# Kernel tuning notes

Hardware: AMD Instinct MI355X
Metric: run time of the kernel (lower is better)

## Reference

```python
import jax, jax.numpy as jnp
import numpy as np
import math


def setup_inputs() -> dict:
    key = jax.random.key(0)
    ks = jax.random.split(key, 8)
    B, L, d_model, d_state, d_conv, expand = 2, 512, 1024, 64, 4, 2
    d_inner = expand * d_model  # 2048
    x = jax.random.normal(ks[0], (B, L, d_model), jnp.float32)
    in_proj_w = jax.random.normal(ks[1], (d_model, 2 * d_inner), jnp.float32) * (d_model ** -0.5)
    conv_w = jax.random.normal(ks[2], (d_inner, 1, d_conv), jnp.float32) * (d_conv ** -0.5)
    conv_b = jnp.zeros((d_inner,), jnp.float32)
    x_proj_w = jax.random.normal(ks[3], (d_inner, 2 * d_state + 1), jnp.float32) * (d_inner ** -0.5)
    dt_w = jax.random.normal(ks[4], (1, d_inner), jnp.float32)
    # dt bias init: softplus^{-1} of dt ~ LogUniform(dt_min, dt_max)
    dt = jnp.exp(jax.random.uniform(ks[5], (d_inner,)) * (math.log(0.1) - math.log(0.001)) + math.log(0.001))
    dt_b = dt + jnp.log(-jnp.expm1(-dt))
    A_log = jnp.broadcast_to(jnp.log(jnp.arange(1, d_state + 1, dtype=jnp.float32)), (d_inner, d_state)) + 0.0
    D = jnp.ones((d_inner,), jnp.float32)
    out_proj_w = jax.random.normal(ks[6], (d_inner, d_model), jnp.float32) * (d_inner ** -0.5)
    return {"x": x, "in_proj_w": in_proj_w, "conv_w": conv_w, "conv_b": conv_b,
            "x_proj_w": x_proj_w, "dt_w": dt_w, "dt_b": dt_b, "A_log": A_log,
            "D": D, "out_proj_w": out_proj_w}


def _mamba_forward(x, in_proj_w, conv_w, conv_b, x_proj_w, dt_w, dt_b, A_log, D, out_proj_w):
    Bsz, L, _ = x.shape
    d_inner, _, K = conv_w.shape
    d_state = A_log.shape[1]
    # in_proj -> split into x-branch and gate z
    xz = x @ in_proj_w                       # (B, L, 2*d_inner)
    xs, z = jnp.split(xz, 2, axis=-1)
    # depthwise causal conv1d (pad K-1 on the left == torch pad both + truncate to L)
    xc = jax.lax.conv_general_dilated(
        xs.transpose(0, 2, 1), conv_w, (1,), [(K - 1, 0)],
        dimension_numbers=("NCH", "OIH", "NCH"), feature_group_count=d_inner)
    xc = xc + conv_b[None, :, None]
    xs = jax.nn.silu(xc.transpose(0, 2, 1))  # (B, L, d_inner)
    # input-dependent SSM params
    xp = xs @ x_proj_w                       # (B, L, 2*d_state + 1)
    Bm = xp[..., :d_state]                   # (B, L, N)
    Cm = xp[..., d_state:2 * d_state]        # (B, L, N)
    dt_raw = xp[..., -1:]                    # (B, L, 1)
    dt = jax.nn.softplus(dt_raw @ dt_w + dt_b)  # (B, L, d_inner)
    A = -jnp.exp(A_log)                      # (d_inner, N)

    def step(state, inp):
        x_t, B_t, C_t, dt_t = inp            # (B,d), (B,N), (B,N), (B,d)
        dA = jnp.exp(dt_t[..., None] * A)    # (B, d, N)
        state = dA * state + (dt_t * x_t)[..., None] * B_t[:, None, :]
        y = jnp.einsum("bdn,bn->bd", state, C_t) + D * x_t
        return state, y

    init = jnp.zeros((Bsz, d_inner, d_state), xs.dtype)
    seq = (xs.transpose(1, 0, 2), Bm.transpose(1, 0, 2),
           Cm.transpose(1, 0, 2), dt.transpose(1, 0, 2))
    new_state, ys = jax.lax.scan(step, init, seq)
    y = ys.transpose(1, 0, 2)                # (B, L, d_inner)
    y = y * jax.nn.silu(z)
    out = y @ out_proj_w                     # (B, L, d_model)
    return out, new_state


def reference(x, in_proj_w, conv_w, conv_b, x_proj_w, dt_w, dt_b, A_log, D, out_proj_w):
    return _mamba_forward(x, in_proj_w, conv_w, conv_b, x_proj_w, dt_w, dt_b, A_log, D, out_proj_w)
```

## Files before the change

kernel.cpp:

```cpp
#include <hip/hip_runtime.h>
#include <hip/hip_bf16.h>


#define N_TOK   1024
#define SEQ_L   512
#define D_MODEL 1024
#define D_INNER 2048
#define D_STATE 64
#define D_XZ    4096
#define N_XP    129

typedef __attribute__((ext_vector_type(8))) short bf16x8;
typedef __attribute__((ext_vector_type(4))) float f32x4;

__device__ __forceinline__ unsigned short f2bf(float f) {
  __hip_bfloat16 h = __float2bfloat16(f);
  return *reinterpret_cast<unsigned short*>(&h);
}
__device__ __forceinline__ float bf16lo(unsigned int u) { return __uint_as_float(u << 16); }
__device__ __forceinline__ float bf16hi(unsigned int u) { return __uint_as_float(u & 0xffff0000u); }

__global__ __launch_bounds__(256) void transpose_bf16(
    const float* __restrict__ src, __hip_bfloat16* __restrict__ dst, int R, int C) {
  __shared__ float t[64][65];
  int c0 = blockIdx.x * 64, r0 = blockIdx.y * 64;
  int tc = threadIdx.x & 63, tg = threadIdx.x >> 6;
#pragma unroll
  for (int i = 0; i < 16; ++i) {
    int r = r0 + tg + i * 4, c = c0 + tc;
    t[tg + i * 4][tc] = (r < R && c < C) ? src[(size_t)r * C + c] : 0.f;
  }
  __syncthreads();
#pragma unroll
  for (int i = 0; i < 16; ++i) {
    int c = c0 + tg + i * 4, r = r0 + tc;
    if (c < C && r < R) dst[(size_t)c * R + r] = __float2bfloat16(t[tc][tg + i * 4]);
  }
}

template<int A_F32>
__global__ __launch_bounds__(256) void gemm_bf16_tn(
    const void* __restrict__ Av, const __hip_bfloat16* __restrict__ Bt,
    float* __restrict__ C, int M, int N, int K) {
  __shared__ short As[128][40];
  __shared__ short Bs[128][40];
  const int brow = blockIdx.y * 128, bcol = blockIdx.x * 128;
  const int tid = threadIdx.x;
  const int lane = tid & 63, wave = tid >> 6;
  const int wm = wave >> 1, wn = wave & 1;
  const int l15 = lane & 15, lk = lane >> 4;
  f32x4 acc[4][4] = {};
  for (int k0 = 0; k0 < K; k0 += 32) {
#pragma unroll
    for (int i = 0; i < 2; ++i) {
      int v = tid + i * 256;
      int r = v >> 2, kc = (v & 3) * 8;
      if (A_F32) {
        const float* Af = (const float*)Av;
        float4 f0 = *(const float4*)&Af[(size_t)(brow + r) * K + k0 + kc];
        float4 f1 = *(const float4*)&Af[(size_t)(brow + r) * K + k0 + kc + 4];
        bf16x8 h;
        h[0] = (short)f2bf(f0.x); h[1] = (short)f2bf(f0.y);
        h[2] = (short)f2bf(f0.z); h[3] = (short)f2bf(f0.w);
        h[4] = (short)f2bf(f1.x); h[5] = (short)f2bf(f1.y);
        h[6] = (short)f2bf(f1.z); h[7] = (short)f2bf(f1.w);
        *(bf16x8*)((char*)&As[0][0] + r * 80 + kc * 2) = h;
      } else {
        const __hip_bfloat16* Ab = (const __hip_bfloat16*)Av;
        *(bf16x8*)((char*)&As[0][0] + r * 80 + kc * 2) =
            *(const bf16x8*)&Ab[(size_t)(brow + r) * K + k0 + kc];
      }
      *(bf16x8*)((char*)&Bs[0][0] + r * 80 + kc * 2) =
          *(const bf16x8*)&Bt[(size_t)(bcol + r) * K + k0 + kc];
    }
    __syncthreads();
    bf16x8 af[4], bfr[4];
#pragma unroll
    for (int m = 0; m < 4; ++m)
      af[m] = *(const bf16x8*)((const char*)&As[0][0] + (wm * 64 + m * 16 + l15) * 80 + lk * 16);
#pragma unroll
    for (int n = 0; n < 4; ++n)
      bfr[n] = *(const bf16x8*)((const char*)&Bs[0][0] + (wn * 64 + n * 16 + l15) * 80 + lk * 16);
#pragma unroll
    for (int m = 0; m < 4; ++m)
#pragma unroll
      for (int n = 0; n < 4; ++n)
        acc[m][n] = __builtin_amdgcn_mfma_f32_16x16x32_bf16(af[m], bfr[n], acc[m][n], 0, 0, 0);
    __syncthreads();
  }
#pragma unroll
  for (int m = 0; m < 4; ++m) {
    int row = brow + wm * 64 + m * 16 + lk * 4;
#pragma unroll
    for (int n = 0; n < 4; ++n) {
      int col = bcol + wn * 64 + n * 16 + l15;
#pragma unroll
      for (int r = 0; r < 4; ++r)
        C[(size_t)(row + r) * N + col] = acc[m][n][r];
    }
  }
}

__global__ __launch_bounds__(256) void gemm_splitk(
    const __hip_bfloat16* __restrict__ A, const __hip_bfloat16* __restrict__ Bt,
    float* __restrict__ P, int M, int N, int K, int kchunk) {
  __shared__ short As[128][40];
  __shared__ short Bs[128][40];
  const int brow = blockIdx.y * 128, bcol = blockIdx.x * 128;
  const int kbase = blockIdx.z * kchunk;
  const int tid = threadIdx.x;
  const int lane = tid & 63, wave = tid >> 6;
  const int wm = wave >> 1, wn = wave & 1;
  const int l15 = lane & 15, lk = lane >> 4;
  f32x4 acc[4][4] = {};
  for (int k0 = kbase; k0 < kbase + kchunk; k0 += 32) {
#pragma unroll
    for (int i = 0; i < 2; ++i) {
      int v = tid + i * 256;
      int r = v >> 2, kc = (v & 3) * 8;
      *(bf16x8*)((char*)&As[0][0] + r * 80 + kc * 2) =
          *(const bf16x8*)&A[(size_t)(brow + r) * K + k0 + kc];
      bf16x8 bv = {};
      if ((bcol + r) < N)
        bv = *(const bf16x8*)&Bt[(size_t)(bcol + r) * K + k0 + kc];
      *(bf16x8*)((char*)&Bs[0][0] + r * 80 + kc * 2) = bv;
    }
    __syncthreads();
    bf16x8 af[4], bfr[4];
#pragma unroll
    for (int m = 0; m < 4; ++m)
      af[m] = *(const bf16x8*)((const char*)&As[0][0] + (wm * 64 + m * 16 + l15) * 80 + lk * 16);
#pragma unroll
    for (int n = 0; n < 4; ++n)
      bfr[n] = *(const bf16x8*)((const char*)&Bs[0][0] + (wn * 64 + n * 16 + l15) * 80 + lk * 16);
#pragma unroll
    for (int m = 0; m < 4; ++m)
#pragma unroll
      for (int n = 0; n < 4; ++n)
        acc[m][n] = __builtin_amdgcn_mfma_f32_16x16x32_bf16(af[m], bfr[n], acc[m][n], 0, 0, 0);
    __syncthreads();
  }
  float* Pz = P + (size_t)blockIdx.z * M * N;
#pragma unroll
  for (int m = 0; m < 4; ++m) {
    int row = brow + wm * 64 + m * 16 + lk * 4;
#pragma unroll
    for (int n = 0; n < 4; ++n) {
      int col = bcol + wn * 64 + n * 16 + l15;
      if (col < N) {
#pragma unroll
        for (int r = 0; r < 4; ++r)
          Pz[(size_t)(row + r) * N + col] = acc[m][n][r];
      }
    }
  }
}

template<int Z>
__global__ __launch_bounds__(256) void reduce_z(
    const float* __restrict__ P, float* __restrict__ out, int n) {
  int i = (blockIdx.x * 256 + threadIdx.x) * 4;
  if (i >= n) return;
  float4 s = *(const float4*)&P[i];
#pragma unroll
  for (int z = 1; z < Z; ++z) {
    float4 v = *(const float4*)&P[(size_t)z * n + i];
    s.x += v.x; s.y += v.y; s.z += v.z; s.w += v.w;
  }
  *(float4*)&out[i] = s;
}

__global__ __launch_bounds__(256) void reduce_bc(
    const float* __restrict__ P, unsigned int* __restrict__ bcP,
    float* __restrict__ dtr) {
  int tok = blockIdx.x * 4 + (threadIdx.x >> 6);
  int n = threadIdx.x & 63;
  const float* p0 = P + (size_t)tok * N_XP + n;
  float sB = 0.f, sC = 0.f;
#pragma unroll
  for (int z = 0; z < 16; ++z) {
    sB += p0[(size_t)z * N_TOK * N_XP];
    sC += p0[(size_t)z * N_TOK * N_XP + 64];
  }
  bcP[(size_t)tok * D_STATE + n] = (unsigned)f2bf(sB) | ((unsigned)f2bf(sC) << 16);
  if (n == 0) {
    float sd = 0.f;
    const float* pd = P + (size_t)tok * N_XP + 128;
#pragma unroll
    for (int z = 0; z < 16; ++z) sd += pd[(size_t)z * N_TOK * N_XP];
    dtr[tok] = sd;
  }
}

__global__ __launch_bounds__(256) void conv_silu_kernel(
    const float* __restrict__ xz, const float* __restrict__ cw,
    const float* __restrict__ cb, float* __restrict__ xc,
    __hip_bfloat16* __restrict__ xcb) {
  int idx = blockIdx.x * 256 + threadIdx.x;
  int c = idx & (D_INNER - 1);
  int tok = idx >> 11;
  int l = tok & (SEQ_L - 1);
  float acc = cb[c];
#pragma unroll
  for (int k = 0; k < 4; ++k) {
    int ll = l - 3 + k;
    if (ll >= 0) acc = fmaf(xz[(size_t)(tok - 3 + k) * D_XZ + c], cw[c * 4 + k], acc);
  }
  float v = acc / (1.f + __expf(-acc));
  xc[idx] = v;
  xcb[idx] = __float2bfloat16(v);
}

__global__ __launch_bounds__(256) void pack_kernel(
    const float* __restrict__ xzf, const float* __restrict__ xc,
    const float* __restrict__ dtr, const float* __restrict__ dt_w,
    const float* __restrict__ dt_b, const float* __restrict__ Dv,
    float2* __restrict__ uaT, unsigned int* __restrict__ ug2) {
  __shared__ float2 la[64][33];
  int tok0 = blockIdx.x * 32, d0 = blockIdx.y * 64;
  int t = threadIdx.x;
  int dl = t & 63, tc = t >> 6;
  int d = d0 + dl;
  float w = dt_w[d], bb = dt_b[d], Dd = Dv[d];
#pragma unroll
  for (int p = 0; p < 8; ++p) {
    int tl = p * 4 + tc;
    int tok = tok0 + tl;
    float xt = xc[(size_t)tok * D_INNER + d];
    float z = xzf[(size_t)tok * D_XZ + D_INNER + d];
    float dt = dtr[tok] * w + bb;
    dt = (dt > 20.f) ? dt : log1pf(__expf(dt));
    la[dl][tl] = make_float2(dt, dt * xt);
    float g = z / (1.f + __expf(-z));
    ug2[(size_t)tok * D_INNER + d] =
        (unsigned int)f2bf(Dd * xt) | ((unsigned int)f2bf(g) << 16);
  }
  __syncthreads();
  int tl2 = t & 31, dg = t >> 5;
#pragma unroll
  for (int q = 0; q < 8; ++q) {
    int dl2 = q * 8 + dg;
    uaT[(size_t)(d0 + dl2) * N_TOK + tok0 + tl2] = la[dl2][tl2];
  }
}

__global__ __launch_bounds__(256) void gate_kernel(
    const float* __restrict__ praw, const unsigned int* __restrict__ ug2,
    __hip_bfloat16* __restrict__ ybb) {
  __shared__ float tile[64][65];
  int tok0 = blockIdx.x * 64, d0 = blockIdx.y * 64;
  int t = threadIdx.x, tc = t & 63, tg = t >> 6;
#pragma unroll
  for (int i = 0; i < 16; ++i) {
    int dl = tg + i * 4;
    tile[dl][tc] = praw[(size_t)(d0 + dl) * N_TOK + tok0 + tc];
  }
  __syncthreads();
#pragma unroll
  for (int i = 0; i < 16; ++i) {
    int tl = tg + i * 4;
    size_t idx = (size_t)(tok0 + tl) * D_INNER + d0 + tc;
    unsigned u = ug2[idx];
    float v = (tile[tc][tl] + bf16lo(u)) * bf16hi(u);
    ybb[idx] = __float2bfloat16(v);
  }
}

template<int CTRL>
__device__ __forceinline__ float dppadd(float v) {
  int t = __builtin_amdgcn_update_dpp(0, __float_as_int(v), CTRL, 0xF, 0xF, true);
  return v + __int_as_float(t);
}
__device__ __forceinline__ float wave_sum64(float v) {
  v = dppadd<0x111>(v);
  v = dppadd<0x112>(v);
  v = dppadd<0x114>(v);
  v = dppadd<0x118>(v);
  v = dppadd<0x142>(v);
  v = dppadd<0x143>(v);
  return v;
}

#define PTOK(dtv, dtxv, bu) { \
    float dA = __expf((dtv) * a); \
    Pr *= dA; \
    s = fmaf(dA, s, (dtxv) * bf16lo(bu)); }

__global__ __launch_bounds__(256) void scan_partial(
    const float2* __restrict__ uaT, const unsigned int* __restrict__ bcP,
    const float* __restrict__ A_log, float* __restrict__ Pp,
    float* __restrict__ sloc) {
  int wid = (blockIdx.x * 256 + threadIdx.x) >> 6;
  int lane = threadIdx.x & 63;
  int ch = wid & 3, d = (wid >> 2) & (D_INNER - 1), b = wid >> 13;
  float a = -__expf(A_log[d * D_STATE + lane]);
  int tok0 = b * SEQ_L + ch * 128;
  const float4* ua = (const float4*)(uaT + (size_t)d * N_TOK + tok0);
  const unsigned* bp = bcP + (size_t)tok0 * D_STATE + lane;
  float s = 0.f, Pr = 1.f;
#pragma unroll 2
  for (int l = 0; l < 128; l += 8) {
    float4 u0 = ua[l / 2], u1 = ua[l / 2 + 1], u2 = ua[l / 2 + 2], u3 = ua[l / 2 + 3];
    unsigned b0 = bp[(l + 0) * 64], b1 = bp[(l + 1) * 64];
    unsigned b2 = bp[(l + 2) * 64], b3 = bp[(l + 3) * 64];
    unsigned b4 = bp[(l + 4) * 64], b5 = bp[(l + 5) * 64];
    unsigned b6 = bp[(l + 6) * 64], b7 = bp[(l + 7) * 64];
    PTOK(u0.x, u0.y, b0) PTOK(u0.z, u0.w, b1)
    PTOK(u1.x, u1.y, b2) PTOK(u1.z, u1.w, b3)
    PTOK(u2.x, u2.y, b4) PTOK(u2.z, u2.w, b5)
    PTOK(u3.x, u3.y, b6) PTOK(u3.z, u3.w, b7)
  }
  Pp[(size_t)wid * D_STATE + lane] = Pr;
  sloc[(size_t)wid * D_STATE + lane] = s;
}

__global__ __launch_bounds__(256) void scan_combine(
    const float* __restrict__ Pp, const float* __restrict__ sloc,
    float* __restrict__ sin, float* __restrict__ state_out) {
  int wid = (blockIdx.x * 256 + threadIdx.x) >> 6;
  int lane = threadIdx.x & 63;
  const float* Pw = Pp + (size_t)wid * 256;
  const float* sw = sloc + (size_t)wid * 256;
  float* si = sin + (size_t)wid * 256;
  float s = 0.f;
  si[lane] = 0.f;
#pragma unroll
  for (int c = 0; c < 4; ++c) {
    s = fmaf(Pw[c * 64 + lane], s, sw[c * 64 + lane]);
    if (c < 3) si[(c + 1) * 64 + lane] = s;
  }
  state_out[(size_t)wid * D_STATE + lane] = s;
}

#define FTOK(dtv, dtxv, bu, pj) { \
    float dA = __expf((dtv) * a); \
    s = fmaf(dA, s, (dtxv) * bf16lo(bu)); \
    pj = wave_sum64(s * bf16hi(bu)); }

__global__ __launch_bounds__(256) void scan_final(
    const float2* __restrict__ uaT, const unsigned int* __restrict__ bcP,
    const float* __restrict__ A_log, const float* __restrict__ sin,
    float* __restrict__ praw) {
  int wid = (blockIdx.x * 256 + threadIdx.x) >> 6;
  int lane = threadIdx.x & 63;
  int ch = wid & 3, d = (wid >> 2) & (D_INNER - 1), b = wid >> 13;
  float a = -__expf(A_log[d * D_STATE + lane]);
  int tok0 = b * SEQ_L + ch * 128;
  const float4* ua = (const float4*)(uaT + (size_t)d * N_TOK + tok0);
  const unsigned* bp = bcP + (size_t)tok0 * D_STATE + lane;
  float* po = praw + (size_t)d * N_TOK + tok0;
  float s = sin[(size_t)wid * D_STATE + lane];
#pragma unroll 2
  for (int l = 0; l < 128; l += 8) {
    float4 u0 = ua[l / 2], u1 = ua[l / 2 + 1], u2 = ua[l / 2 + 2], u3 = ua[l / 2 + 3];
    unsigned b0 = bp[(l + 0) * 64], b1 = bp[(l + 1) * 64];
    unsigned b2 = bp[(l + 2) * 64], b3 = bp[(l + 3) * 64];
    unsigned b4 = bp[(l + 4) * 64], b5 = bp[(l + 5) * 64];
    unsigned b6 = bp[(l + 6) * 64], b7 = bp[(l + 7) * 64];
    float p0, p1, p2, p3, p4, p5, p6, p7;
    FTOK(u0.x, u0.y, b0, p0) FTOK(u0.z, u0.w, b1, p1)
    FTOK(u1.x, u1.y, b2, p2) FTOK(u1.z, u1.w, b3, p3)
    FTOK(u2.x, u2.y, b4, p4) FTOK(u2.z, u2.w, b5, p5)
    FTOK(u3.x, u3.y, b6, p6) FTOK(u3.z, u3.w, b7, p7)
    if (lane == 63) {
      *(float4*)(po + l) = make_float4(p0, p1, p2, p3);
      *(float4*)(po + l + 4) = make_float4(p4, p5, p6, p7);
    }
  }
}

extern "C" void kernel_launch(void* const* d_in, const int* in_sizes, int n_in,
                              void* d_out, int out_size, void* d_ws, size_t ws_size,
                              hipStream_t stream) {
  const float* x         = (const float*)d_in[0];
  const float* in_proj_w = (const float*)d_in[1];
  const float* conv_w    = (const float*)d_in[2];
  const float* conv_b    = (const float*)d_in[3];
  const float* x_proj_w  = (const float*)d_in[4];
  const float* dt_w      = (const float*)d_in[5];
  const float* dt_b      = (const float*)d_in[6];
  const float* A_log     = (const float*)d_in[7];
  const float* Dvec      = (const float*)d_in[8];
  const float* out_proj_w= (const float*)d_in[9];

  char* w = (char*)d_ws;
  __hip_bfloat16* Wt1 = (__hip_bfloat16*)w; w += (size_t)D_XZ * D_MODEL * 2;
  __hip_bfloat16* Wt2 = (__hip_bfloat16*)w; w += (size_t)N_XP * D_INNER * 2;
  __hip_bfloat16* Wt3 = (__hip_bfloat16*)w; w += (size_t)D_MODEL * D_INNER * 2;
  float*          xzf = (float*)w;          w += (size_t)N_TOK * D_XZ * 4;
  float*          xc  = (float*)w;          w += (size_t)N_TOK * D_INNER * 4;
  __hip_bfloat16* xcb = (__hip_bfloat16*)w; w += (size_t)N_TOK * D_INNER * 2;
  float*          P   = (float*)w;          w += (size_t)16 * N_TOK * N_XP * 4;
  unsigned int*   bcP = (unsigned int*)w;   w += (size_t)N_TOK * D_STATE * 4;
  float*          dtr = (float*)w;          w += (size_t)N_TOK * 4;
  float2*         uaT = (float2*)w;         w += (size_t)D_INNER * N_TOK * 8;
  unsigned int*   ug2 = (unsigned int*)w;   w += (size_t)N_TOK * D_INNER * 4;
  float*          praw = P;
  __hip_bfloat16* ybb  = xcb;
  float*          Pp   = xzf;
  float*          sloc = Pp + (size_t)4096 * 256;
  float*          sin  = sloc + (size_t)4096 * 256;
  float*          Pg   = xzf;

  float* out       = (float*)d_out;
  float* state_out = out + (size_t)N_TOK * D_MODEL;

  dim3 blk(256);
  transpose_bf16<<<dim3(D_XZ / 64, D_MODEL / 64), blk, 0, stream>>>(in_proj_w, Wt1, D_MODEL, D_XZ);
  transpose_bf16<<<dim3((N_XP + 63) / 64, D_INNER / 64), blk, 0, stream>>>(x_proj_w, Wt2, D_INNER, N_XP);
  transpose_bf16<<<dim3(D_MODEL / 64, D_INNER / 64), blk, 0, stream>>>(out_proj_w, Wt3, D_INNER, D_MODEL);
  gemm_bf16_tn<1><<<dim3(D_XZ / 128, N_TOK / 128), blk, 0, stream>>>(x, Wt1, xzf, N_TOK, D_XZ, D_MODEL);
  conv_silu_kernel<<<(N_TOK * D_INNER) / 256, blk, 0, stream>>>(xzf, conv_w, conv_b, xc, xcb);
  gemm_splitk<<<dim3((N_XP + 127) / 128, N_TOK / 128, 16), blk, 0, stream>>>(xcb, Wt2, P, N_TOK, N_XP, D_INNER, 128);
  reduce_bc<<<N_TOK / 4, blk, 0, stream>>>(P, bcP, dtr);
  pack_kernel<<<dim3(N_TOK / 32, D_INNER / 64), blk, 0, stream>>>(xzf, xc, dtr, dt_w, dt_b, Dvec, uaT, ug2);
  scan_partial<<<4096, blk, 0, stream>>>(uaT, bcP, A_log, Pp, sloc);
  scan_combine<<<1024, blk, 0, stream>>>(Pp, sloc, sin, state_out);
  scan_final<<<4096, blk, 0, stream>>>(uaT, bcP, A_log, sin, praw);
  gate_kernel<<<dim3(N_TOK / 64, D_INNER / 64), blk, 0, stream>>>(praw, ug2, ybb);
  gemm_splitk<<<dim3(D_MODEL / 128, N_TOK / 128, 4), blk, 0, stream>>>(ybb, Wt3, Pg, N_TOK, D_MODEL, D_INNER, 512);
  reduce_z<4><<<(N_TOK * D_MODEL) / 1024, blk, 0, stream>>>(Pg, out, N_TOK * D_MODEL);
}
```

Before: 328.4 us.

## Fuse chunked scan passes into one kernel and shrink GEMM row tiles

The three scan kernels (partial, combine, final) become one block per (batch, channel). Its four waves each scan a 128-token chunk, combine chunk carries through LDS, then rescan to produce outputs. This removes two launches and the global round-trip of the partial products and states. B/C values are stored interleaved in groups of 8 tokens so each lane loads them as uint4, and the scan loops prefetch the next iteration's data. The GEMMs are templated on row tile size and launched with 64-row tiles to get more blocks, at the cost of less operand reuse per block.

```diff
diff --git a/kernel.cpp b/kernel.cpp
--- a/kernel.cpp
+++ b/kernel.cpp
@@ -38,21 +38,22 @@
   }
 }
 
-template<int A_F32>
+template<int BM, int A_F32>
 __global__ __launch_bounds__(256) void gemm_bf16_tn(
     const void* __restrict__ Av, const __hip_bfloat16* __restrict__ Bt,
     float* __restrict__ C, int M, int N, int K) {
-  __shared__ short As[128][40];
+  const int MF = BM / 32;
+  __shared__ short As[BM][40];
   __shared__ short Bs[128][40];
-  const int brow = blockIdx.y * 128, bcol = blockIdx.x * 128;
+  const int brow = blockIdx.y * BM, bcol = blockIdx.x * 128;
   const int tid = threadIdx.x;
   const int lane = tid & 63, wave = tid >> 6;
   const int wm = wave >> 1, wn = wave & 1;
   const int l15 = lane & 15, lk = lane >> 4;
-  f32x4 acc[4][4] = {};
+  f32x4 acc[MF][4] = {};
   for (int k0 = 0; k0 < K; k0 += 32) {
 #pragma unroll
-    for (int i = 0; i < 2; ++i) {
+    for (int i = 0; i < BM / 64; ++i) {
       int v = tid + i * 256;
       int r = v >> 2, kc = (v & 3) * 8;
       if (A_F32) {
@@ -70,27 +71,32 @@
         *(bf16x8*)((char*)&As[0][0] + r * 80 + kc * 2) =
             *(const bf16x8*)&Ab[(size_t)(brow + r) * K + k0 + kc];
       }
+    }
+#pragma unroll
+    for (int i = 0; i < 2; ++i) {
+      int v = tid + i * 256;
+      int r = v >> 2, kc = (v & 3) * 8;
       *(bf16x8*)((char*)&Bs[0][0] + r * 80 + kc * 2) =
           *(const bf16x8*)&Bt[(size_t)(bcol + r) * K + k0 + kc];
     }
     __syncthreads();
-    bf16x8 af[4], bfr[4];
-#pragma unroll
-    for (int m = 0; m < 4; ++m)
-      af[m] = *(const bf16x8*)((const char*)&As[0][0] + (wm * 64 + m * 16 + l15) * 80 + lk * 16);
+    bf16x8 af[MF], bfr[4];
+#pragma unroll
+    for (int m = 0; m < MF; ++m)
+      af[m] = *(const bf16x8*)((const char*)&As[0][0] + (wm * (BM / 2) + m * 16 + l15) * 80 + lk * 16);
 #pragma unroll
     for (int n = 0; n < 4; ++n)
       bfr[n] = *(const bf16x8*)((const char*)&Bs[0][0] + (wn * 64 + n * 16 + l15) * 80 + lk * 16);
 #pragma unroll
-    for (int m = 0; m < 4; ++m)
+    for (int m = 0; m < MF; ++m)
 #pragma unroll
       for (int n = 0; n < 4; ++n)
         acc[m][n] = __builtin_amdgcn_mfma_f32_16x16x32_bf16(af[m], bfr[n], acc[m][n], 0, 0, 0);
     __syncthreads();
   }
 #pragma unroll
-  for (int m = 0; m < 4; ++m) {
-    int row = brow + wm * 64 + m * 16 + lk * 4;
+  for (int m = 0; m < MF; ++m) {
+    int row = brow + wm * (BM / 2) + m * 16 + lk * 4;
 #pragma unroll
     for (int n = 0; n < 4; ++n) {
       int col = bcol + wn * 64 + n * 16 + l15;
@@ -101,40 +107,47 @@
   }
 }
 
+template<int BM>
 __global__ __launch_bounds__(256) void gemm_splitk(
     const __hip_bfloat16* __restrict__ A, const __hip_bfloat16* __restrict__ Bt,
     float* __restrict__ P, int M, int N, int K, int kchunk) {
-  __shared__ short As[128][40];
+  const int MF = BM / 32;
+  __shared__ short As[BM][40];
   __shared__ short Bs[128][40];
-  const int brow = blockIdx.y * 128, bcol = blockIdx.x * 128;
+  const int brow = blockIdx.y * BM, bcol = blockIdx.x * 128;
   const int kbase = blockIdx.z * kchunk;
   const int tid = threadIdx.x;
   const int lane = tid & 63, wave = tid >> 6;
   const int wm = wave >> 1, wn = wave & 1;
   const int l15 = lane & 15, lk = lane >> 4;
-  f32x4 acc[4][4] = {};
+  f32x4 acc[MF][4] = {};
   for (int k0 = kbase; k0 < kbase + kchunk; k0 += 32) {
 #pragma unroll
-    for (int i = 0; i < 2; ++i) {
+    for (int i = 0; i < BM / 64; ++i) {
       int v = tid + i * 256;
       int r = v >> 2, kc = (v & 3) * 8;
       *(bf16x8*)((char*)&As[0][0] + r * 80 + kc * 2) =
           *(const bf16x8*)&A[(size_t)(brow + r) * K + k0 + kc];
+    }
+#pragma unroll
+    for (int i = 0; i < 2; ++i) {
+      int v = tid + i * 256;
+      int r = v >> 2, kc = (v & 3) * 8;
       bf16x8 bv = {};
       if ((bcol + r) < N)
         bv = *(const bf16x8*)&Bt[(size_t)(bcol + r) * K + k0 + kc];
       *(bf16x8*)((char*)&Bs[0][0] + r * 80 + kc * 2) = bv;
     }
     __syncthreads();
-    bf16x8 af[4], bfr[4];
-#pragma unroll
-    for (int m = 0; m < 4; ++m)
-      af[m] = *(const bf16x8*)((const char*)&As[0][0] + (wm * 64 + m * 16 + l15) * 80 + lk * 16);
+    bf16x8 af[MF], bfr[4];
+#pragma unroll
+    for (int m = 0; m < MF; ++m)
+      af[m] = *(const bf16x8*)((const char*)&As[0][0] + (wm * (BM / 2) + m * 16 + l15) * 80 + lk * 16);
 #pragma unroll
     for (int n = 0; n < 4; ++n)
       bfr[n] = *(const bf16x8*)((const char*)&Bs[0][0] + (wn * 64 + n * 16 + l15) * 80 + lk * 16);
 #pragma unroll
-    for (int m = 0; m < 4; ++m)
+    for (int m = 0; m < MF; ++m)
 #pragma unroll
       for (int n = 0; n < 4; ++n)
         acc[m][n] = __builtin_amdgcn_mfma_f32_16x16x32_bf16(af[m], bfr[n], acc[m][n], 0, 0, 0);
@@ -142,8 +155,8 @@
   }
   float* Pz = P + (size_t)blockIdx.z * M * N;
 #pragma unroll
-  for (int m = 0; m < 4; ++m) {
-    int row = brow + wm * 64 + m * 16 + lk * 4;
+  for (int m = 0; m < MF; ++m) {
+    int row = brow + wm * (BM / 2) + m * 16 + lk * 4;
 #pragma unroll
     for (int n = 0; n < 4; ++n) {
       int col = bcol + wn * 64 + n * 16 + l15;
@@ -171,7 +184,7 @@
 }
 
 __global__ __launch_bounds__(256) void reduce_bc(
-    const float* __restrict__ P, unsigned int* __restrict__ bcP,
+    const float* __restrict__ P, unsigned int* __restrict__ bc8,
     float* __restrict__ dtr) {
   int tok = blockIdx.x * 4 + (threadIdx.x >> 6);
   int n = threadIdx.x & 63;
@@ -182,7 +195,8 @@
     sB += p0[(size_t)z * N_TOK * N_XP];
     sC += p0[(size_t)z * N_TOK * N_XP + 64];
   }
-  bcP[(size_t)tok * D_STATE + n] = (unsigned)f2bf(sB) | ((unsigned)f2bf(sC) << 16);
+  bc8[(size_t)(tok >> 3) * 512 + n * 8 + (tok & 7)] =
+      (unsigned)f2bf(sB) | ((unsigned)f2bf(sC) << 16);
   if (n == 0) {
     float sd = 0.f;
     const float* pd = P + (size_t)tok * N_XP + 128;
@@ -286,85 +300,74 @@
     Pr *= dA; \
     s = fmaf(dA, s, (dtxv) * bf16lo(bu)); }
 
-__global__ __launch_bounds__(256) void scan_partial(
-    const float2* __restrict__ uaT, const unsigned int* __restrict__ bcP,
-    const float* __restrict__ A_log, float* __restrict__ Pp,
-    float* __restrict__ sloc) {
-  int wid = (blockIdx.x * 256 + threadIdx.x) >> 6;
-  int lane = threadIdx.x & 63;
-  int ch = wid & 3, d = (wid >> 2) & (D_INNER - 1), b = wid >> 13;
-  float a = -__expf(A_log[d * D_STATE + lane]);
-  int tok0 = b * SEQ_L + ch * 128;
-  const float4* ua = (const float4*)(uaT + (size_t)d * N_TOK + tok0);
-  const unsigned* bp = bcP + (size_t)tok0 * D_STATE + lane;
-  float s = 0.f, Pr = 1.f;
-#pragma unroll 2
-  for (int l = 0; l < 128; l += 8) {
-    float4 u0 = ua[l / 2], u1 = ua[l / 2 + 1], u2 = ua[l / 2 + 2], u3 = ua[l / 2 + 3];
-    unsigned b0 = bp[(l + 0) * 64], b1 = bp[(l + 1) * 64];
-    unsigned b2 = bp[(l + 2) * 64], b3 = bp[(l + 3) * 64];
-    unsigned b4 = bp[(l + 4) * 64], b5 = bp[(l + 5) * 64];
-    unsigned b6 = bp[(l + 6) * 64], b7 = bp[(l + 7) * 64];
-    PTOK(u0.x, u0.y, b0) PTOK(u0.z, u0.w, b1)
-    PTOK(u1.x, u1.y, b2) PTOK(u1.z, u1.w, b3)
-    PTOK(u2.x, u2.y, b4) PTOK(u2.z, u2.w, b5)
-    PTOK(u3.x, u3.y, b6) PTOK(u3.z, u3.w, b7)
-  }
-  Pp[(size_t)wid * D_STATE + lane] = Pr;
-  sloc[(size_t)wid * D_STATE + lane] = s;
-}
-
-__global__ __launch_bounds__(256) void scan_combine(
-    const float* __restrict__ Pp, const float* __restrict__ sloc,
-    float* __restrict__ sin, float* __restrict__ state_out) {
-  int wid = (blockIdx.x * 256 + threadIdx.x) >> 6;
-  int lane = threadIdx.x & 63;
-  const float* Pw = Pp + (size_t)wid * 256;
-  const float* sw = sloc + (size_t)wid * 256;
-  float* si = sin + (size_t)wid * 256;
-  float s = 0.f;
-  si[lane] = 0.f;
-#pragma unroll
-  for (int c = 0; c < 4; ++c) {
-    s = fmaf(Pw[c * 64 + lane], s, sw[c * 64 + lane]);
-    if (c < 3) si[(c + 1) * 64 + lane] = s;
-  }
-  state_out[(size_t)wid * D_STATE + lane] = s;
-}
-
 #define FTOK(dtv, dtxv, bu, pj) { \
     float dA = __expf((dtv) * a); \
     s = fmaf(dA, s, (dtxv) * bf16lo(bu)); \
     pj = wave_sum64(s * bf16hi(bu)); }
 
-__global__ __launch_bounds__(256) void scan_final(
-    const float2* __restrict__ uaT, const unsigned int* __restrict__ bcP,
-    const float* __restrict__ A_log, const float* __restrict__ sin,
-    float* __restrict__ praw) {
-  int wid = (blockIdx.x * 256 + threadIdx.x) >> 6;
-  int lane = threadIdx.x & 63;
-  int ch = wid & 3, d = (wid >> 2) & (D_INNER - 1), b = wid >> 13;
+__global__ __launch_bounds__(256) void scan_fused(
+    const float2* __restrict__ uaT, const unsigned int* __restrict__ bc8,
+    const float* __restrict__ A_log, float* __restrict__ praw,
+    float* __restrict__ state_out) {
+  __shared__ float lP[4][64], lS[4][64];
+  int bd = blockIdx.x;
+  int d = bd & (D_INNER - 1), b = bd >> 11;
+  int ch = threadIdx.x >> 6, lane = threadIdx.x & 63;
   float a = -__expf(A_log[d * D_STATE + lane]);
   int tok0 = b * SEQ_L + ch * 128;
-  const float4* ua = (const float4*)(uaT + (size_t)d * N_TOK + tok0);
-  const unsigned* bp = bcP + (size_t)tok0 * D_STATE + lane;
-  float* po = praw + (size_t)d * N_TOK + tok0;
-  float s = sin[(size_t)wid * D_STATE + lane];
-#pragma unroll 2
-  for (int l = 0; l < 128; l += 8) {
-    float4 u0 = ua[l / 2], u1 = ua[l / 2 + 1], u2 = ua[l / 2 + 2], u3 = ua[l / 2 + 3];
-    unsigned b0 = bp[(l + 0) * 64], b1 = bp[(l + 1) * 64];
-    unsigned b2 = bp[(l + 2) * 64], b3 = bp[(l + 3) * 64];
-    unsigned b4 = bp[(l + 4) * 64], b5 = bp[(l + 5) * 64];
-    unsigned b6 = bp[(l + 6) * 64], b7 = bp[(l + 7) * 64];
-    float p0, p1, p2, p3, p4, p5, p6, p7;
-    FTOK(u0.x, u0.y, b0, p0) FTOK(u0.z, u0.w, b1, p1)
-    FTOK(u1.x, u1.y, b2, p2) FTOK(u1.z, u1.w, b3, p3)
-    FTOK(u2.x, u2.y, b4, p4) FTOK(u2.z, u2.w, b5, p5)
-    FTOK(u3.x, u3.y, b6, p6) FTOK(u3.z, u3.w, b7, p7)
-    if (lane == 63) {
-      *(float4*)(po + l) = make_float4(p0, p1, p2, p3);
-      *(float4*)(po + l + 4) = make_float4(p4, p5, p6, p7);
+  const float4* uq0 = (const float4*)(uaT + (size_t)d * N_TOK + tok0);
+  const uint4* bq0 = (const uint4*)bc8 + (size_t)(tok0 >> 3) * 128 + lane * 2;
+
+  float s = 0.f, Pr = 1.f;
+  {
+    const float4* uq = uq0; const uint4* bq = bq0;
+    uint4 q0 = bq[0], q1 = bq[1];
+    float4 u0 = uq[0], u1 = uq[1], u2 = uq[2], u3 = uq[3];
+#pragma unroll 1
+    for (int it = 0; it < 16; ++it) {
+      bq += 128; uq += 4;
+      uint4 nq0 = bq[0], nq1 = bq[1];
+      float4 nu0 = uq[0], nu1 = uq[1];
+      float4 nu2 = uq[2], nu3 = uq[3];
+      PTOK(u0.x, u0.y, q0.x) PTOK(u0.z, u0.w, q0.y)
+      PTOK(u1.x, u1.y, q0.z) PTOK(u1.z, u1.w, q0.w)
+      PTOK(u2.x, u2.y, q1.x) PTOK(u2.z, u2.w, q1.y)
+      PTOK(u3.x, u3.y, q1.z) PTOK(u3.z, u3.w, q1.w)
+      q0 = nq0; q1 = nq1; u0 = nu0; u1 = nu1; u2 = nu2; u3 = nu3;
+    }
+  }
+  lP[ch][lane] = Pr; lS[ch][lane] = s;
+  __syncthreads();
+  float sin = 0.f;
+#pragma unroll
+  for (int c = 0; c < 3; ++c)
+    if (c < ch) sin = fmaf(lP[c][lane], sin, lS[c][lane]);
+  if (ch == 3)
+    state_out[(size_t)bd * D_STATE + lane] = fmaf(lP[3][lane], sin, lS[3][lane]);
+
+  s = sin;
+  {
+    const float4* uq = uq0; const uint4* bq = bq0;
+    float* po = praw + (size_t)d * N_TOK + tok0;
+    uint4 q0 = bq[0], q1 = bq[1];
+    float4 u0 = uq[0], u1 = uq[1], u2 = uq[2], u3 = uq[3];
+#pragma unroll 1
+    for (int it = 0; it < 16; ++it) {
+      bq += 128; uq += 4;
+      uint4 nq0 = bq[0], nq1 = bq[1];
+      float4 nu0 = uq[0], nu1 = uq[1];
+      float4 nu2 = uq[2], nu3 = uq[3];
+      float p0, p1, p2, p3, p4, p5, p6, p7;
+      FTOK(u0.x, u0.y, q0.x, p0) FTOK(u0.z, u0.w, q0.y, p1)
+      FTOK(u1.x, u1.y, q0.z, p2) FTOK(u1.z, u1.w, q0.w, p3)
+      FTOK(u2.x, u2.y, q1.x, p4) FTOK(u2.z, u2.w, q1.y, p5)
+      FTOK(u3.x, u3.y, q1.z, p6) FTOK(u3.z, u3.w, q1.w, p7)
+      if (lane == 63) {
+        *(float4*)(po) = make_float4(p0, p1, p2, p3);
+        *(float4*)(po + 4) = make_float4(p4, p5, p6, p7);
+      }
+      po += 8;
+      q0 = nq0; q1 = nq1; u0 = nu0; u1 = nu1; u2 = nu2; u3 = nu3;
     }
   }
 }
@@ -391,15 +394,12 @@
   float*          xc  = (float*)w;          w += (size_t)N_TOK * D_INNER * 4;
   __hip_bfloat16* xcb = (__hip_bfloat16*)w; w += (size_t)N_TOK * D_INNER * 2;
   float*          P   = (float*)w;          w += (size_t)16 * N_TOK * N_XP * 4;
-  unsigned int*   bcP = (unsigned int*)w;   w += (size_t)N_TOK * D_STATE * 4;
+  unsigned int*   bc8 = (unsigned int*)w;   w += (size_t)N_TOK * D_STATE * 4;
   float*          dtr = (float*)w;          w += (size_t)N_TOK * 4;
   float2*         uaT = (float2*)w;         w += (size_t)D_INNER * N_TOK * 8;
   unsigned int*   ug2 = (unsigned int*)w;   w += (size_t)N_TOK * D_INNER * 4;
   float*          praw = P;
   __hip_bfloat16* ybb  = xcb;
-  float*          Pp   = xzf;
-  float*          sloc = Pp + (size_t)4096 * 256;
-  float*          sin  = sloc + (size_t)4096 * 256;
   float*          Pg   = xzf;
 
   float* out       = (float*)d_out;
@@ -409,15 +409,13 @@
   transpose_bf16<<<dim3(D_XZ / 64, D_MODEL / 64), blk, 0, stream>>>(in_proj_w, Wt1, D_MODEL, D_XZ);
   transpose_bf16<<<dim3((N_XP + 63) / 64, D_INNER / 64), blk, 0, stream>>>(x_proj_w, Wt2, D_INNER, N_XP);
   transpose_bf16<<<dim3(D_MODEL / 64, D_INNER / 64), blk, 0, stream>>>(out_proj_w, Wt3, D_INNER, D_MODEL);
-  gemm_bf16_tn<1><<<dim3(D_XZ / 128, N_TOK / 128), blk, 0, stream>>>(x, Wt1, xzf, N_TOK, D_XZ, D_MODEL);
+  gemm_bf16_tn<64, 1><<<dim3(D_XZ / 128, N_TOK / 64), blk, 0, stream>>>(x, Wt1, xzf, N_TOK, D_XZ, D_MODEL);
   conv_silu_kernel<<<(N_TOK * D_INNER) / 256, blk, 0, stream>>>(xzf, conv_w, conv_b, xc, xcb);
-  gemm_splitk<<<dim3((N_XP + 127) / 128, N_TOK / 128, 16), blk, 0, stream>>>(xcb, Wt2, P, N_TOK, N_XP, D_INNER, 128);
-  reduce_bc<<<N_TOK / 4, blk, 0, stream>>>(P, bcP, dtr);
+  gemm_splitk<64><<<dim3((N_XP + 127) / 128, N_TOK / 64, 16), blk, 0, stream>>>(xcb, Wt2, P, N_TOK, N_XP, D_INNER, 128);
+  reduce_bc<<<N_TOK / 4, blk, 0, stream>>>(P, bc8, dtr);
   pack_kernel<<<dim3(N_TOK / 32, D_INNER / 64), blk, 0, stream>>>(xzf, xc, dtr, dt_w, dt_b, Dvec, uaT, ug2);
-  scan_partial<<<4096, blk, 0, stream>>>(uaT, bcP, A_log, Pp, sloc);
-  scan_combine<<<1024, blk, 0, stream>>>(Pp, sloc, sin, state_out);
-  scan_final<<<4096, blk, 0, stream>>>(uaT, bcP, A_log, sin, praw);
+  scan_fused<<<2 * D_INNER, blk, 0, stream>>>(uaT, bc8, A_log, praw, state_out);
   gate_kernel<<<dim3(N_TOK / 64, D_INNER / 64), blk, 0, stream>>>(praw, ug2, ybb);
-  gemm_splitk<<<dim3(D_MODEL / 128, N_TOK / 128, 4), blk, 0, stream>>>(ybb, Wt3, Pg, N_TOK, D_MODEL, D_INNER, 512);
+  gemm_splitk<64><<<dim3(D_MODEL / 128, N_TOK / 64, 4), blk, 0, stream>>>(ybb, Wt3, Pg, N_TOK, D_MODEL, D_INNER, 512);
   reduce_z<4><<<(N_TOK * D_MODEL) / 1024, blk, 0, stream>>>(Pg, out, N_TOK * D_MODEL);
 }
```

Result: faster. 318.1 us (-3.1%).
